# Kernel optimization log

Hardware: AMD Instinct MI355X
Metric: run time of the kernel (lower is better)

## Reference

```python
import jax, jax.numpy as jnp
import numpy as np


def setup_inputs() -> dict:
    key = jax.random.key(0)
    ks = jax.random.split(key, 6)
    B, N_in, N_out, D_in, D_out, S = 64, 195, 778, 256, 128, 9
    nnz = 3 * N_out
    x = jax.random.normal(ks[0], (B, N_in, D_in), dtype=jnp.float32)
    # upsample transform: each output vertex receives 3 weighted source verts
    row = jnp.repeat(jnp.arange(N_out, dtype=jnp.int64), 3)
    col = jax.random.randint(ks[1], (nnz,), 0, N_in).astype(jnp.int64)
    value = jax.random.uniform(ks[2], (nnz,), dtype=jnp.float32)
    indices = jax.random.randint(ks[3], (N_out, S), 0, N_out).astype(jnp.int64)
    W = jax.random.normal(ks[4], (D_in * S, D_out), dtype=jnp.float32) * 0.02
    b = jnp.zeros((D_out,), dtype=jnp.float32)
    return {"x": x, "row": row, "col": col, "value": value,
            "indices": indices, "W": W, "b": b}


def reference(x, row, col, value, indices, W, b):
    B, N_in, D = x.shape
    N_out, S = indices.shape
    # Pool: gather source verts, scale by barycentric weight, scatter-add
    msg = x[:, col, :] * value[None, :, None]                # (B, nnz, D)
    pooled = jnp.zeros((B, N_out, D), x.dtype).at[:, row, :].add(msg)
    # SpiralConv: gather spiral neighborhood, flatten, linear
    g = pooled[:, indices.reshape(-1), :].reshape(B, N_out, S * D)
    out = jnp.einsum('bnk,ko->bno', g, W) + b                # (B, N_out, D_out)
    return jax.nn.relu(out)
```

## Files before the change

### kernel.cpp

```cpp
#include <hip/hip_runtime.h>
#include <hip/hip_bf16.h>
#include <stdint.h>

#define NB 64
#define N_IN 195
#define N_OUT 778
#define D_IN 256
#define D_OUTC 128
#define NS 9
#define KTOT 2304
#define MM 49792
#define BM 128
#define BK 64

using short8 = __attribute__((ext_vector_type(8))) short;
using f32x4  = __attribute__((ext_vector_type(4))) float;

__device__ __forceinline__ void gload16(const void* g, void* l) {
  __builtin_amdgcn_global_load_lds(
      (const __attribute__((address_space(1))) uint32_t*)g,
      (__attribute__((address_space(3))) uint32_t*)l, 16, 0, 0);
}

__global__ __launch_bounds__(256) void pool_kernel(
    const float* __restrict__ x, const int* __restrict__ col,
    const float* __restrict__ value, __hip_bfloat16* __restrict__ pooled) {
  int m = blockIdx.x * 2 + (threadIdx.x >> 7);
  int t = threadIdx.x & 127;
  int b = (unsigned)m / N_OUT;
  int n = m - b * N_OUT;
  int j = 3 * n;
  int c0 = col[j], c1 = col[j + 1], c2 = col[j + 2];
  float v0 = value[j], v1 = value[j + 1], v2 = value[j + 2];
  const float2* x0 = (const float2*)(x + ((size_t)b * N_IN + c0) * D_IN);
  const float2* x1 = (const float2*)(x + ((size_t)b * N_IN + c1) * D_IN);
  const float2* x2 = (const float2*)(x + ((size_t)b * N_IN + c2) * D_IN);
  float2 a0 = x0[t], a1 = x1[t], a2 = x2[t];
  float r0 = v0 * a0.x + v1 * a1.x + v2 * a2.x;
  float r1 = v0 * a0.y + v1 * a1.y + v2 * a2.y;
  __hip_bfloat162 pk;
  pk.x = __float2bfloat16(r0);
  pk.y = __float2bfloat16(r1);
  ((__hip_bfloat162*)(pooled + (size_t)m * D_IN))[t] = pk;
}

__global__ __launch_bounds__(256) void wt_kernel(
    const float* __restrict__ W, __hip_bfloat16* __restrict__ Wt) {
  int idx = blockIdx.x * 256 + threadIdx.x;
  int o = idx / KTOT, k = idx - o * KTOT;
  Wt[idx] = __float2bfloat16(W[(size_t)k * D_OUTC + o]);
}

__global__ __launch_bounds__(256) void gemm_kernel(
    const __hip_bfloat16* __restrict__ pooled,
    const __hip_bfloat16* __restrict__ Wt,
    const int* __restrict__ indices,
    const float* __restrict__ bias,
    float* __restrict__ out) {
  __shared__ __hip_bfloat16 Asm[BM * BK];
  __shared__ __hip_bfloat16 Bsm[D_OUTC * BK];

  const int tid  = threadIdx.x;
  const int wave = tid >> 6;
  const int lane = tid & 63;
  const int bm   = blockIdx.x * BM;
  const int wr = wave >> 1, wc = wave & 1;
  const int srow = lane >> 3, schunk = lane & 7;

  int n_i[4], b778_i[4], ax_i[4];
  const __hip_bfloat16* wtb_i[4];
  #pragma unroll
  for (int i = 0; i < 4; ++i) {
    int r = (wave * 4 + i) * 8 + srow;
    int m = bm + r;
    int b = (unsigned)m / N_OUT;
    int n = m - b * N_OUT;
    n_i[i] = n;
    b778_i[i] = b * N_OUT;
    ax_i[i] = (schunk ^ (r & 7)) * 8;
    wtb_i[i] = Wt + (size_t)r * KTOT + (size_t)((schunk ^ (r & 7)) * 8);
  }

  f32x4 acc[4][4];
  #pragma unroll
  for (int i = 0; i < 4; ++i)
    #pragma unroll
    for (int j = 0; j < 4; ++j)
      acc[i][j] = f32x4{0.f, 0.f, 0.f, 0.f};

  char* AsmB = (char*)Asm;
  char* BsmB = (char*)Bsm;

  for (int s0 = 0; s0 < NS; ++s0) {
    int gi[4];
    #pragma unroll
    for (int i = 0; i < 4; ++i) gi[i] = indices[n_i[i] * NS + s0];
    #pragma unroll
    for (int q = 0; q < 4; ++q) {
      const int d0 = q * 64;
      const int k0 = s0 * 256 + d0;
      #pragma unroll
      for (int i = 0; i < 4; ++i) {
        const __hip_bfloat16* srcA =
            pooled + ((size_t)(b778_i[i] + gi[i]) * D_IN + d0 + ax_i[i]);
        gload16(srcA, AsmB + (size_t)(wave * 4 + i) * 1024);
        const __hip_bfloat16* srcB = wtb_i[i] + k0;
        gload16(srcB, BsmB + (size_t)(wave * 4 + i) * 1024);
      }
      __syncthreads();
      #pragma unroll
      for (int h = 0; h < 2; ++h) {
        short8 af[4], bf[4];
        const int cb = h * 64 + (lane >> 4) * 16;
        #pragma unroll
        for (int i = 0; i < 4; ++i) {
          int r = wr * 64 + i * 16 + (lane & 15);
          af[i] = *(const short8*)(AsmB + r * 128 + (cb ^ ((r & 7) << 4)));
        }
        #pragma unroll
        for (int j = 0; j < 4; ++j) {
          int o = wc * 64 + j * 16 + (lane & 15);
          bf[j] = *(const short8*)(BsmB + o * 128 + (cb ^ ((o & 7) << 4)));
        }
        #pragma unroll
        for (int i = 0; i < 4; ++i)
          #pragma unroll
          for (int j = 0; j < 4; ++j)
            acc[i][j] = __builtin_amdgcn_mfma_f32_16x16x32_bf16(
                af[i], bf[j], acc[i][j], 0, 0, 0);
      }
      __syncthreads();
    }
  }

  #pragma unroll
  for (int j = 0; j < 4; ++j) {
    int colo = wc * 64 + j * 16 + (lane & 15);
    float bo = bias[colo];
    #pragma unroll
    for (int i = 0; i < 4; ++i) {
      #pragma unroll
      for (int qq = 0; qq < 4; ++qq) {
        int row = bm + wr * 64 + i * 16 + (lane >> 4) * 4 + qq;
        float v = acc[i][j][qq] + bo;
        out[(size_t)row * D_OUTC + colo] = fmaxf(v, 0.f);
      }
    }
  }
}

extern "C" void kernel_launch(void* const* d_in, const int* in_sizes, int n_in,
                              void* d_out, int out_size, void* d_ws, size_t ws_size,
                              hipStream_t stream) {
  const float* x       = (const float*)d_in[0];
  const int*   col     = (const int*)d_in[2];
  const float* value   = (const float*)d_in[3];
  const int*   indices = (const int*)d_in[4];
  const float* W       = (const float*)d_in[5];
  const float* bias    = (const float*)d_in[6];
  float* out           = (float*)d_out;

  __hip_bfloat16* pooled = (__hip_bfloat16*)d_ws;
  __hip_bfloat16* Wt = (__hip_bfloat16*)((char*)d_ws + (size_t)MM * D_IN * 2);

  pool_kernel<<<MM / 2, 256, 0, stream>>>(x, col, value, pooled);
  wt_kernel<<<(D_OUTC * KTOT) / 256, 256, 0, stream>>>(W, Wt);
  gemm_kernel<<<MM / BM, 256, 0, stream>>>(pooled, Wt, indices, bias, out);
}
```

Before: 74.06 us.

## Double-buffer GEMM LDS loads, remap workgroups per XCD, merge prep kernels

```diff
diff --git a/kernel.cpp b/kernel.cpp
--- a/kernel.cpp
+++ b/kernel.cpp
@@ -12,6 +12,9 @@
 #define MM 49792
 #define BM 128
 #define BK 64
+#define NWG (MM / BM)
+#define POOL_BLOCKS (MM / 2)
+#define WT_BLOCKS ((D_OUTC * KTOT) / 256)
 
 using short8 = __attribute__((ext_vector_type(8))) short;
 using f32x4  = __attribute__((ext_vector_type(4))) float;
@@ -22,33 +25,34 @@
       (__attribute__((address_space(3))) uint32_t*)l, 16, 0, 0);
 }
 
-__global__ __launch_bounds__(256) void pool_kernel(
+__global__ __launch_bounds__(256) void prep_kernel(
     const float* __restrict__ x, const int* __restrict__ col,
-    const float* __restrict__ value, __hip_bfloat16* __restrict__ pooled) {
-  int m = blockIdx.x * 2 + (threadIdx.x >> 7);
-  int t = threadIdx.x & 127;
-  int b = (unsigned)m / N_OUT;
-  int n = m - b * N_OUT;
-  int j = 3 * n;
-  int c0 = col[j], c1 = col[j + 1], c2 = col[j + 2];
-  float v0 = value[j], v1 = value[j + 1], v2 = value[j + 2];
-  const float2* x0 = (const float2*)(x + ((size_t)b * N_IN + c0) * D_IN);
-  const float2* x1 = (const float2*)(x + ((size_t)b * N_IN + c1) * D_IN);
-  const float2* x2 = (const float2*)(x + ((size_t)b * N_IN + c2) * D_IN);
-  float2 a0 = x0[t], a1 = x1[t], a2 = x2[t];
-  float r0 = v0 * a0.x + v1 * a1.x + v2 * a2.x;
-  float r1 = v0 * a0.y + v1 * a1.y + v2 * a2.y;
-  __hip_bfloat162 pk;
-  pk.x = __float2bfloat16(r0);
-  pk.y = __float2bfloat16(r1);
-  ((__hip_bfloat162*)(pooled + (size_t)m * D_IN))[t] = pk;
-}
-
-__global__ __launch_bounds__(256) void wt_kernel(
-    const float* __restrict__ W, __hip_bfloat16* __restrict__ Wt) {
-  int idx = blockIdx.x * 256 + threadIdx.x;
-  int o = idx / KTOT, k = idx - o * KTOT;
-  Wt[idx] = __float2bfloat16(W[(size_t)k * D_OUTC + o]);
+    const float* __restrict__ value, const float* __restrict__ W,
+    __hip_bfloat16* __restrict__ pooled, __hip_bfloat16* __restrict__ Wt) {
+  int bid = blockIdx.x;
+  if (bid < POOL_BLOCKS) {
+    int m = bid * 2 + (threadIdx.x >> 7);
+    int t = threadIdx.x & 127;
+    int b = (unsigned)m / N_OUT;
+    int n = m - b * N_OUT;
+    int j = 3 * n;
+    int c0 = col[j], c1 = col[j + 1], c2 = col[j + 2];
+    float v0 = value[j], v1 = value[j + 1], v2 = value[j + 2];
+    const float2* x0 = (const float2*)(x + ((size_t)b * N_IN + c0) * D_IN);
+    const float2* x1 = (const float2*)(x + ((size_t)b * N_IN + c1) * D_IN);
+    const float2* x2 = (const float2*)(x + ((size_t)b * N_IN + c2) * D_IN);
+    float2 a0 = x0[t], a1 = x1[t], a2 = x2[t];
+    float r0 = v0 * a0.x + v1 * a1.x + v2 * a2.x;
+    float r1 = v0 * a0.y + v1 * a1.y + v2 * a2.y;
+    __hip_bfloat162 pk;
+    pk.x = __float2bfloat16(r0);
+    pk.y = __float2bfloat16(r1);
+    ((__hip_bfloat162*)(pooled + (size_t)m * D_IN))[t] = pk;
+  } else {
+    int idx = (bid - POOL_BLOCKS) * 256 + threadIdx.x;
+    int o = idx / KTOT, k = idx - o * KTOT;
+    Wt[idx] = __float2bfloat16(W[(size_t)k * D_OUTC + o]);
+  }
 }
 
 __global__ __launch_bounds__(256) void gemm_kernel(
@@ -57,15 +61,22 @@
     const int* __restrict__ indices,
     const float* __restrict__ bias,
     float* __restrict__ out) {
-  __shared__ __hip_bfloat16 Asm[BM * BK];
-  __shared__ __hip_bfloat16 Bsm[D_OUTC * BK];
+  __shared__ __hip_bfloat16 Asm[2][BM * BK];
+  __shared__ __hip_bfloat16 Bsm[2][D_OUTC * BK];
 
   const int tid  = threadIdx.x;
   const int wave = tid >> 6;
   const int lane = tid & 63;
-  const int bm   = blockIdx.x * BM;
   const int wr = wave >> 1, wc = wave & 1;
   const int srow = lane >> 3, schunk = lane & 7;
+
+  {
+  }
+  const int bidr = blockIdx.x;
+  const int xcd = bidr & 7, loc = bidr >> 3;
+  const int q8 = NWG >> 3, r8 = NWG & 7;
+  const int wg = (xcd < r8 ? xcd * (q8 + 1) : r8 * (q8 + 1) + (xcd - r8) * q8) + loc;
+  const int bm = wg * BM;
 
   int n_i[4], b778_i[4], ax_i[4];
   const __hip_bfloat16* wtb_i[4];
@@ -88,48 +99,70 @@
     for (int j = 0; j < 4; ++j)
       acc[i][j] = f32x4{0.f, 0.f, 0.f, 0.f};
 
-  char* AsmB = (char*)Asm;
-  char* BsmB = (char*)Bsm;
+  char* AsmB = (char*)&Asm[0][0];
+  char* BsmB = (char*)&Bsm[0][0];
+
+  auto stage = [&](int buf, int d0, int k0, const int* gi) {
+    #pragma unroll
+    for (int i = 0; i < 4; ++i) {
+      const __hip_bfloat16* srcA =
+          pooled + ((size_t)(b778_i[i] + gi[i]) * D_IN + d0 + ax_i[i]);
+      gload16(srcA, AsmB + buf * 16384 + (wave * 4 + i) * 1024);
+      const __hip_bfloat16* srcB = wtb_i[i] + k0;
+      gload16(srcB, BsmB + buf * 16384 + (wave * 4 + i) * 1024);
+    }
+  };
+
+  auto compute = [&](int buf) {
+    const char* Ab = AsmB + buf * 16384;
+    const char* Bb = BsmB + buf * 16384;
+    #pragma unroll
+    for (int h = 0; h < 2; ++h) {
+      short8 af[4], bf[4];
+      const int cb = h * 64 + (lane >> 4) * 16;
+      #pragma unroll
+      for (int i = 0; i < 4; ++i) {
+        int r = wr * 64 + i * 16 + (lane & 15);
+        af[i] = *(const short8*)(Ab + r * 128 + (cb ^ ((r & 7) << 4)));
+      }
+      #pragma unroll
+      for (int j = 0; j < 4; ++j) {
+        int o = wc * 64 + j * 16 + (lane & 15);
+        bf[j] = *(const short8*)(Bb + o * 128 + (cb ^ ((o & 7) << 4)));
+      }
+      #pragma unroll
+      for (int i = 0; i < 4; ++i)
+        #pragma unroll
+        for (int j = 0; j < 4; ++j)
+          acc[i][j] = __builtin_amdgcn_mfma_f32_16x16x32_bf16(
+              af[i], bf[j], acc[i][j], 0, 0, 0);
+    }
+  };
+
+  int giA[4], giB[4];
+  #pragma unroll
+  for (int i = 0; i < 4; ++i) giA[i] = indices[n_i[i] * NS + 0];
+  stage(0, 0, 0, giA);
+  __syncthreads();
 
   for (int s0 = 0; s0 < NS; ++s0) {
-    int gi[4];
-    #pragma unroll
-    for (int i = 0; i < 4; ++i) gi[i] = indices[n_i[i] * NS + s0];
+    if (s0 < NS - 1) {
+      #pragma unroll
+      for (int i = 0; i < 4; ++i) giB[i] = indices[n_i[i] * NS + s0 + 1];
+    }
     #pragma unroll
     for (int q = 0; q < 4; ++q) {
-      const int d0 = q * 64;
-      const int k0 = s0 * 256 + d0;
-      #pragma unroll
-      for (int i = 0; i < 4; ++i) {
-        const __hip_bfloat16* srcA =
-            pooled + ((size_t)(b778_i[i] + gi[i]) * D_IN + d0 + ax_i[i]);
-        gload16(srcA, AsmB + (size_t)(wave * 4 + i) * 1024);
-        const __hip_bfloat16* srcB = wtb_i[i] + k0;
-        gload16(srcB, BsmB + (size_t)(wave * 4 + i) * 1024);
-      }
+      if (q < 3) {
+        stage((q & 1) ^ 1, (q + 1) * 64, s0 * 256 + (q + 1) * 64, giA);
+      } else if (s0 < NS - 1) {
+        stage((q & 1) ^ 1, 0, (s0 + 1) * 256, giB);
+      }
+      compute(q & 1);
       __syncthreads();
-      #pragma unroll
-      for (int h = 0; h < 2; ++h) {
-        short8 af[4], bf[4];
-        const int cb = h * 64 + (lane >> 4) * 16;
-        #pragma unroll
-        for (int i = 0; i < 4; ++i) {
-          int r = wr * 64 + i * 16 + (lane & 15);
-          af[i] = *(const short8*)(AsmB + r * 128 + (cb ^ ((r & 7) << 4)));
-        }
-        #pragma unroll
-        for (int j = 0; j < 4; ++j) {
-          int o = wc * 64 + j * 16 + (lane & 15);
-          bf[j] = *(const short8*)(BsmB + o * 128 + (cb ^ ((o & 7) << 4)));
-        }
-        #pragma unroll
-        for (int i = 0; i < 4; ++i)
-          #pragma unroll
-          for (int j = 0; j < 4; ++j)
-            acc[i][j] = __builtin_amdgcn_mfma_f32_16x16x32_bf16(
-                af[i], bf[j], acc[i][j], 0, 0, 0);
-      }
-      __syncthreads();
+    }
+    if (s0 < NS - 1) {
+      #pragma unroll
+      for (int i = 0; i < 4; ++i) giA[i] = giB[i];
     }
   }
 
@@ -163,7 +196,7 @@
   __hip_bfloat16* pooled = (__hip_bfloat16*)d_ws;
   __hip_bfloat16* Wt = (__hip_bfloat16*)((char*)d_ws + (size_t)MM * D_IN * 2);
 
-  pool_kernel<<<MM / 2, 256, 0, stream>>>(x, col, value, pooled);
-  wt_kernel<<<(D_OUTC * KTOT) / 256, 256, 0, stream>>>(W, Wt);
-  gemm_kernel<<<MM / BM, 256, 0, stream>>>(pooled, Wt, indices, bias, out);
-}
+  prep_kernel<<<POOL_BLOCKS + WT_BLOCKS, 256, 0, stream>>>(x, col, value, W,
+                                                           pooled, Wt);
+  gemm_kernel<<<NWG, 256, 0, stream>>>(pooled, Wt, indices, bias, out);
+}
```

Measured after the change: 72.71 us. No clear change (-1.8%).
